# Performance work log

Measured on AMD Instinct MI355X. Metric: run time of the kernel, lower is better.

The kernel has to match this reference:

```python
import jax, jax.numpy as jnp
import numpy as np

B_SZ, T_A, T_B, EMB, HID = 16, 1024, 1024, 768, 1024

def setup_inputs() -> dict:
    key = jax.random.key(0)
    kA, kB, k1, k2 = jax.random.split(key, 4)
    s1 = 1.0 / np.sqrt(EMB)
    s2 = 1.0 / np.sqrt(HID)
    return {
        "A": jax.random.normal(kA, (B_SZ, T_A, EMB), jnp.float32),
        "B": jax.random.normal(kB, (B_SZ, T_B, EMB), jnp.float32),
        "W1": jax.random.normal(k1, (EMB, HID), jnp.float32) * s1,
        "b1": jnp.zeros((HID,), jnp.float32),
        "W2": jax.random.normal(k2, (HID, HID), jnp.float32) * s2,
        "b2": jnp.zeros((HID,), jnp.float32),
    }

def _mlp(x, W1, b1, W2, b2):
    # Linear -> ReLU -> Linear -> ReLU (dropout omitted / eval mode)
    h = jax.nn.relu(x @ W1 + b1)
    return jax.nn.relu(h @ W2 + b2)

def reference(A, B, W1, b1, W2, b2):
    f_A = _mlp(A, W1, b1, W2, b2)             # (bs, ta, h)
    f_B = _mlp(B, W1, b1, W2, b2)             # (bs, tb, h)
    e = jnp.einsum("bah,bch->bac", f_A, f_B)  # (bs, ta, tb)
    beta = jnp.einsum("bac,bce->bae", jax.nn.softmax(e, axis=-1), B)
    alpha = jnp.einsum("bca,bae->bce",
                       jax.nn.softmax(e, axis=1).transpose(0, 2, 1)[:, :, :] * 1.0,
                       A) if False else jnp.einsum(
        "bca,bae->bce", jax.nn.softmax(e.transpose(0, 2, 1), axis=-1), A)
    return beta, alpha
```

## Files before the change

kernel.cpp:

```cpp
#include <hip/hip_runtime.h>
#include <cstdint>


#define L2E 1.4426950408889634f

typedef _Float16 half8 __attribute__((ext_vector_type(8)));
typedef _Float16 half4v __attribute__((ext_vector_type(4)));
typedef float f32x4 __attribute__((ext_vector_type(4)));

__device__ __forceinline__ void gl_lds16(const void* g, void* l) {
  __builtin_amdgcn_global_load_lds(
      (const __attribute__((address_space(1))) unsigned int*)g,
      (__attribute__((address_space(3))) unsigned int*)l, 16, 0, 0);
}

template<int K, bool BIASRELU, bool STATS, typename OutT>
__global__ __launch_bounds__(256, 2)
void gemm_k(const _Float16* __restrict__ X, const _Float16* __restrict__ Y,
            const float* __restrict__ bias, OutT* __restrict__ C, int N,
            long xbs, long ybs, long cbs, int gm, int gn, int gz,
            float* __restrict__ prm, float* __restrict__ prs,
            float* __restrict__ pcm, float* __restrict__ pcs)
{
  __shared__ __align__(16) _Float16 sA[128 * 32];
  __shared__ __align__(16) _Float16 sB[128 * 32];
  const int t = threadIdx.x;
  const int lane = t & 63, w = t >> 6;
  const int wr = w >> 1, wc = w & 1;
  const int lm = lane & 15, lk = (lane >> 4) * 8;

  const int id = blockIdx.x;
  const int c = id & 7, s = id >> 3;
  int m, n, bz;
  if (gz == 1) {
    int q = s / gn;
    n = s - q * gn;
    m = c * (gm >> 3) + q;
    bz = 0;
  } else {
    int tpb = gm * gn;
    int bq = s / tpb;
    bz = c * (gz >> 3) + bq;
    int r = s - bq * tpb;
    int mq = r / gn;
    m = mq;
    n = r - mq * gn;
  }
  const int m0 = m * 128, n0 = n * 128;

  X += (size_t)bz * xbs;
  Y += (size_t)bz * ybs;
  C += (size_t)bz * cbs;

  f32x4 acc[4][4] = {};

  for (int kt = 0; kt < K; kt += 32) {
    __syncthreads();
#pragma unroll
    for (int r = 0; r < 2; ++r) {
      int cid = r * 256 + t;
      int row = cid >> 2, c8 = (cid & 3) * 8;
      gl_lds16(X + (size_t)(m0 + row) * K + kt + c8, sA + cid * 8);
    }
#pragma unroll
    for (int r = 0; r < 2; ++r) {
      int cid = r * 256 + t;
      int row = cid >> 2, c8 = (cid & 3) * 8;
      gl_lds16(Y + (size_t)(n0 + row) * K + kt + c8, sB + cid * 8);
    }
    __syncthreads();

    half8 af[4], bf[4];
#pragma unroll
    for (int mi = 0; mi < 4; ++mi)
      af[mi] = *(const half8*)(sA + (wr * 64 + mi * 16 + lm) * 32 + lk);
#pragma unroll
    for (int ni = 0; ni < 4; ++ni)
      bf[ni] = *(const half8*)(sB + (wc * 64 + ni * 16 + lm) * 32 + lk);
#pragma unroll
    for (int mi = 0; mi < 4; ++mi)
#pragma unroll
      for (int ni = 0; ni < 4; ++ni)
        acc[mi][ni] = __builtin_amdgcn_mfma_f32_16x16x32_f16(af[mi], bf[ni], acc[mi][ni], 0, 0, 0);
  }

#pragma unroll
  for (int mi = 0; mi < 4; ++mi) {
    const int rbase = m0 + wr * 64 + mi * 16 + (lane >> 4) * 4;
#pragma unroll
    for (int ni = 0; ni < 4; ++ni) {
      const int col = n0 + wc * 64 + ni * 16 + lm;
      float bv = 0.f;
      if constexpr (BIASRELU) bv = bias[col];
#pragma unroll
      for (int q = 0; q < 4; ++q) {
        float v = acc[mi][ni][q] + bv;
        if constexpr (BIASRELU) v = fmaxf(v, 0.f);
        C[(size_t)(rbase + q) * N + col] = (OutT)v;
      }
    }
  }

  if constexpr (STATS) {
    __shared__ float sRm[256], sRs[256], sCm[256], sCs[256];
    float rowm[4][4], rows_[4][4];
#pragma unroll
    for (int mi = 0; mi < 4; ++mi) {
#pragma unroll
      for (int q = 0; q < 4; ++q) {
        float mloc = fmaxf(fmaxf(acc[mi][0][q], acc[mi][1][q]),
                           fmaxf(acc[mi][2][q], acc[mi][3][q]));
#pragma unroll
        for (int msk = 1; msk < 16; msk <<= 1)
          mloc = fmaxf(mloc, __shfl_xor(mloc, msk));
        float sl = 0.f;
#pragma unroll
        for (int ni = 0; ni < 4; ++ni)
          sl += exp2f((acc[mi][ni][q] - mloc) * L2E);
#pragma unroll
        for (int msk = 1; msk < 16; msk <<= 1)
          sl += __shfl_xor(sl, msk);
        rowm[mi][q] = mloc;
        rows_[mi][q] = sl;
      }
    }
    if (lm == 0) {
#pragma unroll
      for (int mi = 0; mi < 4; ++mi)
#pragma unroll
        for (int q = 0; q < 4; ++q) {
          int rloc = wr * 64 + mi * 16 + (lane >> 4) * 4 + q;
          sRm[wc * 128 + rloc] = rowm[mi][q];
          sRs[wc * 128 + rloc] = rows_[mi][q];
        }
    }
#pragma unroll
    for (int ni = 0; ni < 4; ++ni) {
      float mloc = -3.0e38f;
#pragma unroll
      for (int mi = 0; mi < 4; ++mi)
#pragma unroll
        for (int q = 0; q < 4; ++q)
          mloc = fmaxf(mloc, acc[mi][ni][q]);
      mloc = fmaxf(mloc, __shfl_xor(mloc, 16));
      mloc = fmaxf(mloc, __shfl_xor(mloc, 32));
      float sl = 0.f;
#pragma unroll
      for (int mi = 0; mi < 4; ++mi)
#pragma unroll
        for (int q = 0; q < 4; ++q)
          sl += exp2f((acc[mi][ni][q] - mloc) * L2E);
      sl += __shfl_xor(sl, 16);
      sl += __shfl_xor(sl, 32);
      if ((lane >> 4) == 0) {
        int cloc = wc * 64 + ni * 16 + lm;
        sCm[wr * 128 + cloc] = mloc;
        sCs[wr * 128 + cloc] = sl;
      }
    }
    __syncthreads();
    if (t < 128) {
      float m1 = sRm[t], m2 = sRm[128 + t];
      float M = fmaxf(m1, m2);
      float S = sRs[t] * exp2f((m1 - M) * L2E) + sRs[128 + t] * exp2f((m2 - M) * L2E);
      size_t o = ((size_t)bz * 8 + n) * 1024 + m0 + t;
      prm[o] = M;
      prs[o] = S;
    } else {
      int u = t - 128;
      float m1 = sCm[u], m2 = sCm[128 + u];
      float M = fmaxf(m1, m2);
      float S = sCs[u] * exp2f((m1 - M) * L2E) + sCs[128 + u] * exp2f((m2 - M) * L2E);
      size_t o = ((size_t)bz * 8 + m) * 1024 + n0 + u;
      pcm[o] = M;
      pcs[o] = S;
    }
  }
}

__global__ __launch_bounds__(256)
void stats_combine(const float* __restrict__ prm, const float* __restrict__ prs,
                   const float* __restrict__ pcm, const float* __restrict__ pcs,
                   float* __restrict__ rm, float* __restrict__ ri,
                   float* __restrict__ cm, float* __restrict__ ci)
{
  int idx = blockIdx.x * 256 + threadIdx.x;
  int bz = idx >> 10, pos = idx & 1023;
  const float* pm = blockIdx.y ? pcm : prm;
  const float* ps = blockIdx.y ? pcs : prs;
  float mj[8], sj[8];
#pragma unroll
  for (int j = 0; j < 8; ++j) {
    size_t o = ((size_t)bz * 8 + j) * 1024 + pos;
    mj[j] = pm[o];
    sj[j] = ps[o];
  }
  float M = -3.0e38f;
#pragma unroll
  for (int j = 0; j < 8; ++j) M = fmaxf(M, mj[j]);
  float S = 0.f;
#pragma unroll
  for (int j = 0; j < 8; ++j) S += sj[j] * exp2f((mj[j] - M) * L2E);
  float* om = blockIdx.y ? cm : rm;
  float* oi = blockIdx.y ? ci : ri;
  om[idx] = M;
  oi[idx] = 1.f / S;
}

__global__ __launch_bounds__(256)
void softmax_apply(const float* __restrict__ e,
                   const float* __restrict__ rm, const float* __restrict__ ri,
                   const float* __restrict__ cm, const float* __restrict__ ci,
                   _Float16* __restrict__ P, _Float16* __restrict__ PT)
{
  __shared__ _Float16 tl[64][65];
  const int bz = blockIdx.z;
  const int r0 = blockIdx.y * 64, c0 = blockIdx.x * 64;
  const size_t bo = (size_t)bz * 1048576;
  const int t = threadIdx.x;
#pragma unroll
  for (int p = 0; p < 4; ++p) {
    int idx = p * 256 + t;
    int row = idx >> 4, col4 = (idx & 15) * 4;
    float4 v = *(const float4*)(e + bo + (size_t)(r0 + row) * 1024 + c0 + col4);
    float vv[4] = {v.x, v.y, v.z, v.w};
    const float mrow = rm[bz * 1024 + r0 + row];
    const float irow = ri[bz * 1024 + r0 + row];
    half4v op;
#pragma unroll
    for (int j = 0; j < 4; ++j) {
      op[j] = (_Float16)(exp2f((vv[j] - mrow) * L2E) * irow);
      float mcol = cm[bz * 1024 + c0 + col4 + j];
      float icol = ci[bz * 1024 + c0 + col4 + j];
      tl[col4 + j][row] = (_Float16)(exp2f((vv[j] - mcol) * L2E) * icol);
    }
    *(half4v*)(P + bo + (size_t)(r0 + row) * 1024 + c0 + col4) = op;
  }
  __syncthreads();
#pragma unroll
  for (int p = 0; p < 4; ++p) {
    int idx = p * 256 + t;
    int trow = idx >> 4, tcol4 = (idx & 15) * 4;
    half4v ov;
#pragma unroll
    for (int j = 0; j < 4; ++j) ov[j] = tl[trow][tcol4 + j];
    *(half4v*)(PT + bo + (size_t)(c0 + trow) * 1024 + r0 + tcol4) = ov;
  }
}

__global__ __launch_bounds__(256)
void transpose_cvt(const float* __restrict__ in, _Float16* __restrict__ out, int R, int C)
{
  __shared__ float tl[32][33];
  const size_t bo = (size_t)blockIdx.z * R * C;
  int x = blockIdx.x * 32 + threadIdx.x;
  int y0 = blockIdx.y * 32;
  for (int i = threadIdx.y; i < 32; i += 8)
    tl[i][threadIdx.x] = in[bo + (size_t)(y0 + i) * C + x];
  __syncthreads();
  int xo = y0 + threadIdx.x;
  int c0 = blockIdx.x * 32;
  for (int i = threadIdx.y; i < 32; i += 8)
    out[bo + (size_t)(c0 + i) * R + xo] = (_Float16)tl[threadIdx.x][i];
}

__global__ __launch_bounds__(256)
void cvt_f16(const float* __restrict__ in, _Float16* __restrict__ out, int n4)
{
  int i = blockIdx.x * 256 + threadIdx.x;
  if (i >= n4) return;
  float4 v = ((const float4*)in)[i];
  half4v o;
  o[0] = (_Float16)v.x; o[1] = (_Float16)v.y; o[2] = (_Float16)v.z; o[3] = (_Float16)v.w;
  ((half4v*)out)[i] = o;
}

extern "C" void kernel_launch(void* const* d_in, const int* in_sizes, int n_in,
                              void* d_out, int out_size, void* d_ws, size_t ws_size,
                              hipStream_t stream)
{
  const float* A  = (const float*)d_in[0];
  const float* B  = (const float*)d_in[1];
  const float* W1 = (const float*)d_in[2];
  const float* b1 = (const float*)d_in[3];
  const float* W2 = (const float*)d_in[4];
  const float* b2 = (const float*)d_in[5];
  float* out = (float*)d_out;

  char* ws = (char*)d_ws;
  _Float16* Af  = (_Float16*)(ws + 0);
  _Float16* Bf  = (_Float16*)(ws + 25165824);
  _Float16* W1t = (_Float16*)(ws + 50331648);
  _Float16* W2t = (_Float16*)(ws + 51904512);
  float*    prm = (float*)   (ws + 50331648);
  float*    prs = (float*)   (ws + 50331648 + 524288);
  float*    pcm = (float*)   (ws + 50331648 + 1048576);
  float*    pcs = (float*)   (ws + 50331648 + 1572864);
  _Float16* fAB = (_Float16*)(ws + 54001664);
  _Float16* P   = (_Float16*)(ws + 54001664);
  _Float16* PT  = (_Float16*)(ws + 87556096);
  _Float16* h   = (_Float16*)(ws + 121110528);
  float*    e   = (float*)   (ws + 121110528);
  float*    me  = (float*)   (ws + 188219392);
  float*    ie  = (float*)   (ws + 188219392 + 65536);
  float*    mc  = (float*)   (ws + 188219392 + 131072);
  float*    ic  = (float*)   (ws + 188219392 + 196608);
  _Float16* fA = fAB;
  _Float16* fB = fAB + 16777216;
  _Float16* At = Af;
  _Float16* Bt = Bf;

  dim3 blk(256);
  dim3 tblk(32, 8);

  cvt_f16<<<12288, blk, 0, stream>>>(A, Af, 3145728);
  cvt_f16<<<12288, blk, 0, stream>>>(B, Bf, 3145728);
  transpose_cvt<<<dim3(32, 24, 1), tblk, 0, stream>>>(W1, W1t, 768, 1024);
  transpose_cvt<<<dim3(32, 32, 1), tblk, 0, stream>>>(W2, W2t, 1024, 1024);

  gemm_k<768, true, false, _Float16><<<2048, blk, 0, stream>>>(
      Af, W1t, b1, h, 1024, 0, 0, 0, 256, 8, 1,
      nullptr, nullptr, nullptr, nullptr);
  transpose_cvt<<<dim3(24, 32, 16), tblk, 0, stream>>>(A, At, 1024, 768);
  transpose_cvt<<<dim3(24, 32, 16), tblk, 0, stream>>>(B, Bt, 1024, 768);
  gemm_k<1024, true, false, _Float16><<<2048, blk, 0, stream>>>(
      h, W2t, b2, fAB, 1024, 0, 0, 0, 256, 8, 1,
      nullptr, nullptr, nullptr, nullptr);

  gemm_k<1024, false, true, float><<<1024, blk, 0, stream>>>(
      fA, fB, nullptr, e, 1024, 1048576L, 1048576L, 1048576L, 8, 8, 16,
      prm, prs, pcm, pcs);

  stats_combine<<<dim3(64, 2), blk, 0, stream>>>(prm, prs, pcm, pcs, me, ie, mc, ic);

  softmax_apply<<<dim3(16, 16, 16), blk, 0, stream>>>(e, me, ie, mc, ic, P, PT);

  gemm_k<1024, false, false, float><<<768, blk, 0, stream>>>(
      P, Bt, nullptr, out, 768, 1048576L, 786432L, 786432L, 8, 6, 16,
      nullptr, nullptr, nullptr, nullptr);
  gemm_k<1024, false, false, float><<<768, blk, 0, stream>>>(
      PT, At, nullptr, out + 12582912, 768, 1048576L, 786432L, 786432L, 8, 6, 16,
      nullptr, nullptr, nullptr, nullptr);
}
```

Measured before the change: 540.0 us.

## Double GEMM K-tile with swizzled LDS, fuse stats into softmax, merge launches

Result: faster. 502.4 us (-7.0%).

```diff
diff --git a/kernel.cpp b/kernel.cpp
--- a/kernel.cpp
+++ b/kernel.cpp
@@ -20,17 +20,22 @@
             const float* __restrict__ bias, OutT* __restrict__ C, int N,
             long xbs, long ybs, long cbs, int gm, int gn, int gz,
             float* __restrict__ prm, float* __restrict__ prs,
-            float* __restrict__ pcm, float* __restrict__ pcs)
-{
-  __shared__ __align__(16) _Float16 sA[128 * 32];
-  __shared__ __align__(16) _Float16 sB[128 * 32];
+            float* __restrict__ pcm, float* __restrict__ pcs,
+            const _Float16* __restrict__ X2, const _Float16* __restrict__ Y2,
+            OutT* __restrict__ C2, int shalf)
+{
+  __shared__ __align__(16) _Float16 sA[128 * 64];
+  __shared__ __align__(16) _Float16 sB[128 * 64];
   const int t = threadIdx.x;
   const int lane = t & 63, w = t >> 6;
   const int wr = w >> 1, wc = w & 1;
-  const int lm = lane & 15, lk = (lane >> 4) * 8;
+  const int lm = lane & 15, g = lane >> 4;
+  const int xr = lane & 7;
 
   const int id = blockIdx.x;
-  const int c = id & 7, s = id >> 3;
+  const int c = id & 7;
+  int s = id >> 3;
+  if (shalf && s >= shalf) { s -= shalf; X = X2; Y = Y2; C = C2; }
   int m, n, bz;
   if (gz == 1) {
     int q = s / gn;
@@ -42,9 +47,8 @@
     int bq = s / tpb;
     bz = c * (gz >> 3) + bq;
     int r = s - bq * tpb;
-    int mq = r / gn;
-    m = mq;
-    n = r - mq * gn;
+    m = r / gn;
+    n = r - m * gn;
   }
   const int m0 = m * 128, n0 = n * 128;
 
@@ -52,36 +56,49 @@
   Y += (size_t)bz * ybs;
   C += (size_t)bz * cbs;
 
+  const int stg_row = t >> 3;
+  const int stg_koff = (((t & 7) ^ ((t >> 3) & 7)) << 3);
+
+  int arow[4], brow[4], axo[2];
+#pragma unroll
+  for (int i = 0; i < 4; ++i) {
+    arow[i] = (wr * 64 + i * 16 + lm) * 64;
+    brow[i] = (wc * 64 + i * 16 + lm) * 64;
+  }
+  axo[0] = ((0 * 4 + g) ^ xr) * 8;
+  axo[1] = ((1 * 4 + g) ^ xr) * 8;
+
   f32x4 acc[4][4] = {};
 
-  for (int kt = 0; kt < K; kt += 32) {
+  for (int kt = 0; kt < K; kt += 64) {
     __syncthreads();
 #pragma unroll
-    for (int r = 0; r < 2; ++r) {
-      int cid = r * 256 + t;
-      int row = cid >> 2, c8 = (cid & 3) * 8;
-      gl_lds16(X + (size_t)(m0 + row) * K + kt + c8, sA + cid * 8);
-    }
-#pragma unroll
-    for (int r = 0; r < 2; ++r) {
-      int cid = r * 256 + t;
-      int row = cid >> 2, c8 = (cid & 3) * 8;
-      gl_lds16(Y + (size_t)(n0 + row) * K + kt + c8, sB + cid * 8);
+    for (int r = 0; r < 4; ++r) {
+      int row = r * 32 + stg_row;
+      gl_lds16(X + (size_t)(m0 + row) * K + kt + stg_koff, sA + (r * 256 + t) * 8);
+    }
+#pragma unroll
+    for (int r = 0; r < 4; ++r) {
+      int row = r * 32 + stg_row;
+      gl_lds16(Y + (size_t)(n0 + row) * K + kt + stg_koff, sB + (r * 256 + t) * 8);
     }
     __syncthreads();
 
     half8 af[4], bf[4];
 #pragma unroll
-    for (int mi = 0; mi < 4; ++mi)
-      af[mi] = *(const half8*)(sA + (wr * 64 + mi * 16 + lm) * 32 + lk);
-#pragma unroll
-    for (int ni = 0; ni < 4; ++ni)
-      bf[ni] = *(const half8*)(sB + (wc * 64 + ni * 16 + lm) * 32 + lk);
-#pragma unroll
-    for (int mi = 0; mi < 4; ++mi)
+    for (int ks = 0; ks < 2; ++ks) {
+#pragma unroll
+      for (int mi = 0; mi < 4; ++mi)
+        af[mi] = *(const half8*)(sA + arow[mi] + axo[ks]);
 #pragma unroll
       for (int ni = 0; ni < 4; ++ni)
-        acc[mi][ni] = __builtin_amdgcn_mfma_f32_16x16x32_f16(af[mi], bf[ni], acc[mi][ni], 0, 0, 0);
+        bf[ni] = *(const half8*)(sB + brow[ni] + axo[ks]);
+#pragma unroll
+      for (int mi = 0; mi < 4; ++mi)
+#pragma unroll
+        for (int ni = 0; ni < 4; ++ni)
+          acc[mi][ni] = __builtin_amdgcn_mfma_f32_16x16x32_f16(af[mi], bf[ni], acc[mi][ni], 0, 0, 0);
+    }
   }
 
 #pragma unroll
@@ -179,60 +196,55 @@
 }
 
 __global__ __launch_bounds__(256)
-void stats_combine(const float* __restrict__ prm, const float* __restrict__ prs,
+void softmax_apply(const float* __restrict__ e,
+                   const float* __restrict__ prm, const float* __restrict__ prs,
                    const float* __restrict__ pcm, const float* __restrict__ pcs,
-                   float* __restrict__ rm, float* __restrict__ ri,
-                   float* __restrict__ cm, float* __restrict__ ci)
-{
-  int idx = blockIdx.x * 256 + threadIdx.x;
-  int bz = idx >> 10, pos = idx & 1023;
-  const float* pm = blockIdx.y ? pcm : prm;
-  const float* ps = blockIdx.y ? pcs : prs;
-  float mj[8], sj[8];
-#pragma unroll
-  for (int j = 0; j < 8; ++j) {
-    size_t o = ((size_t)bz * 8 + j) * 1024 + pos;
-    mj[j] = pm[o];
-    sj[j] = ps[o];
-  }
-  float M = -3.0e38f;
-#pragma unroll
-  for (int j = 0; j < 8; ++j) M = fmaxf(M, mj[j]);
-  float S = 0.f;
-#pragma unroll
-  for (int j = 0; j < 8; ++j) S += sj[j] * exp2f((mj[j] - M) * L2E);
-  float* om = blockIdx.y ? cm : rm;
-  float* oi = blockIdx.y ? ci : ri;
-  om[idx] = M;
-  oi[idx] = 1.f / S;
-}
-
-__global__ __launch_bounds__(256)
-void softmax_apply(const float* __restrict__ e,
-                   const float* __restrict__ rm, const float* __restrict__ ri,
-                   const float* __restrict__ cm, const float* __restrict__ ci,
                    _Float16* __restrict__ P, _Float16* __restrict__ PT)
 {
   __shared__ _Float16 tl[64][65];
+  __shared__ float sRm[64], sRi[64], sCm[64], sCi[64];
   const int bz = blockIdx.z;
   const int r0 = blockIdx.y * 64, c0 = blockIdx.x * 64;
   const size_t bo = (size_t)bz * 1048576;
   const int t = threadIdx.x;
+
+  if (t < 128) {
+    const int isCol = t >> 6;
+    const int u = t & 63;
+    const float* pm = isCol ? pcm : prm;
+    const float* ps = isCol ? pcs : prs;
+    const int pos = (isCol ? c0 : r0) + u;
+    float mj[8], sj[8];
+#pragma unroll
+    for (int j = 0; j < 8; ++j) {
+      size_t o = ((size_t)bz * 8 + j) * 1024 + pos;
+      mj[j] = pm[o];
+      sj[j] = ps[o];
+    }
+    float M = -3.0e38f;
+#pragma unroll
+    for (int j = 0; j < 8; ++j) M = fmaxf(M, mj[j]);
+    float S = 0.f;
+#pragma unroll
+    for (int j = 0; j < 8; ++j) S += sj[j] * exp2f((mj[j] - M) * L2E);
+    if (isCol) { sCm[u] = M; sCi[u] = 1.f / S; }
+    else       { sRm[u] = M; sRi[u] = 1.f / S; }
+  }
+  __syncthreads();
+
 #pragma unroll
   for (int p = 0; p < 4; ++p) {
     int idx = p * 256 + t;
     int row = idx >> 4, col4 = (idx & 15) * 4;
     float4 v = *(const float4*)(e + bo + (size_t)(r0 + row) * 1024 + c0 + col4);
     float vv[4] = {v.x, v.y, v.z, v.w};
-    const float mrow = rm[bz * 1024 + r0 + row];
-    const float irow = ri[bz * 1024 + r0 + row];
+    const float mrow = sRm[row];
+    const float irow = sRi[row];
     half4v op;
 #pragma unroll
     for (int j = 0; j < 4; ++j) {
       op[j] = (_Float16)(exp2f((vv[j] - mrow) * L2E) * irow);
-      float mcol = cm[bz * 1024 + c0 + col4 + j];
-      float icol = ci[bz * 1024 + c0 + col4 + j];
-      tl[col4 + j][row] = (_Float16)(exp2f((vv[j] - mcol) * L2E) * icol);
+      tl[col4 + j][row] = (_Float16)(exp2f((vv[j] - sCm[col4 + j]) * L2E) * sCi[col4 + j]);
     }
     *(half4v*)(P + bo + (size_t)(r0 + row) * 1024 + c0 + col4) = op;
   }
@@ -249,10 +261,16 @@
 }
 
 __global__ __launch_bounds__(256)
-void transpose_cvt(const float* __restrict__ in, _Float16* __restrict__ out, int R, int C)
+void transpose_cvt(const float* __restrict__ in1, _Float16* __restrict__ out1,
+                   const float* __restrict__ in2, _Float16* __restrict__ out2,
+                   int R, int C, int nb)
 {
   __shared__ float tl[32][33];
-  const size_t bo = (size_t)blockIdx.z * R * C;
+  int z = blockIdx.z;
+  const float* in = in1;
+  _Float16* out = out1;
+  if (z >= nb) { z -= nb; in = in2; out = out2; }
+  const size_t bo = (size_t)z * R * C;
   int x = blockIdx.x * 32 + threadIdx.x;
   int y0 = blockIdx.y * 32;
   for (int i = threadIdx.y; i < 32; i += 8)
@@ -265,10 +283,13 @@
 }
 
 __global__ __launch_bounds__(256)
-void cvt_f16(const float* __restrict__ in, _Float16* __restrict__ out, int n4)
+void cvt_f16_2(const float* __restrict__ inA, const float* __restrict__ inB,
+               _Float16* __restrict__ oA, _Float16* __restrict__ oB, int n4)
 {
   int i = blockIdx.x * 256 + threadIdx.x;
-  if (i >= n4) return;
+  const float* in = inA;
+  _Float16* out = oA;
+  if (i >= n4) { i -= n4; in = inB; out = oB; }
   float4 v = ((const float4*)in)[i];
   half4v o;
   o[0] = (_Float16)v.x; o[1] = (_Float16)v.y; o[2] = (_Float16)v.z; o[3] = (_Float16)v.w;
@@ -301,10 +322,6 @@
   _Float16* PT  = (_Float16*)(ws + 87556096);
   _Float16* h   = (_Float16*)(ws + 121110528);
   float*    e   = (float*)   (ws + 121110528);
-  float*    me  = (float*)   (ws + 188219392);
-  float*    ie  = (float*)   (ws + 188219392 + 65536);
-  float*    mc  = (float*)   (ws + 188219392 + 131072);
-  float*    ic  = (float*)   (ws + 188219392 + 196608);
   _Float16* fA = fAB;
   _Float16* fB = fAB + 16777216;
   _Float16* At = Af;
@@ -313,32 +330,25 @@
   dim3 blk(256);
   dim3 tblk(32, 8);
 
-  cvt_f16<<<12288, blk, 0, stream>>>(A, Af, 3145728);
-  cvt_f16<<<12288, blk, 0, stream>>>(B, Bf, 3145728);
-  transpose_cvt<<<dim3(32, 24, 1), tblk, 0, stream>>>(W1, W1t, 768, 1024);
-  transpose_cvt<<<dim3(32, 32, 1), tblk, 0, stream>>>(W2, W2t, 1024, 1024);
+  cvt_f16_2<<<24576, blk, 0, stream>>>(A, B, Af, Bf, 3145728);
+  transpose_cvt<<<dim3(32, 24, 1), tblk, 0, stream>>>(W1, W1t, nullptr, nullptr, 768, 1024, 1);
+  transpose_cvt<<<dim3(32, 32, 1), tblk, 0, stream>>>(W2, W2t, nullptr, nullptr, 1024, 1024, 1);
 
   gemm_k<768, true, false, _Float16><<<2048, blk, 0, stream>>>(
       Af, W1t, b1, h, 1024, 0, 0, 0, 256, 8, 1,
-      nullptr, nullptr, nullptr, nullptr);
-  transpose_cvt<<<dim3(24, 32, 16), tblk, 0, stream>>>(A, At, 1024, 768);
-  transpose_cvt<<<dim3(24, 32, 16), tblk, 0, stream>>>(B, Bt, 1024, 768);
+      nullptr, nullptr, nullptr, nullptr, nullptr, nullptr, nullptr, 0);
+  transpose_cvt<<<dim3(24, 32, 32), tblk, 0, stream>>>(A, At, B, Bt, 1024, 768, 16);
   gemm_k<1024, true, false, _Float16><<<2048, blk, 0, stream>>>(
       h, W2t, b2, fAB, 1024, 0, 0, 0, 256, 8, 1,
-      nullptr, nullptr, nullptr, nullptr);
+      nullptr, nullptr, nullptr, nullptr, nullptr, nullptr, nullptr, 0);
 
   gemm_k<1024, false, true, float><<<1024, blk, 0, stream>>>(
       fA, fB, nullptr, e, 1024, 1048576L, 1048576L, 1048576L, 8, 8, 16,
-      prm, prs, pcm, pcs);
-
-  stats_combine<<<dim3(64, 2), blk, 0, stream>>>(prm, prs, pcm, pcs, me, ie, mc, ic);
-
-  softmax_apply<<<dim3(16, 16, 16), blk, 0, stream>>>(e, me, ie, mc, ic, P, PT);
-
-  gemm_k<1024, false, false, float><<<768, blk, 0, stream>>>(
+      prm, prs, pcm, pcs, nullptr, nullptr, nullptr, 0);
+
+  softmax_apply<<<dim3(16, 16, 16), blk, 0, stream>>>(e, prm, prs, pcm, pcs, P, PT);
+
+  gemm_k<1024, false, false, float><<<1536, blk, 0, stream>>>(
       P, Bt, nullptr, out, 768, 1048576L, 786432L, 786432L, 8, 6, 16,
-      nullptr, nullptr, nullptr, nullptr);
-  gemm_k<1024, false, false, float><<<768, blk, 0, stream>>>(
-      PT, At, nullptr, out + 12582912, 768, 1048576L, 786432L, 786432L, 8, 6, 16,
-      nullptr, nullptr, nullptr, nullptr);
-}
+      nullptr, nullptr, nullptr, nullptr, PT, At, out + 12582912, 96);
+}
```
